# Optimization experiments

Measured on AMD Instinct MI355X. Metric: run time of the kernel, lower is better.

Reference implementation:

```python
import math
import jax, jax.numpy as jnp
import numpy as np

B, S, HID = 1, 256, 1024
H, D = 16, 64
INV_NORM = 1.0 / math.sqrt(D)  # inv_norm_factor (beta = 1.0)
NEG = -1e9


def _bloom_alibi(num_heads, seq_len):
    # standard Bloom alibi slopes, shape [H, 1, S]
    closest_pow2 = 2 ** math.floor(math.log2(num_heads))
    base = 2.0 ** (-(2.0 ** -(math.log2(closest_pow2) - 3)))
    slopes = base ** np.arange(1, closest_pow2 + 1)
    if closest_pow2 != num_heads:
        extra_base = 2.0 ** (-(2.0 ** -(math.log2(2 * closest_pow2) - 3)))
        n_extra = min(closest_pow2, num_heads - closest_pow2)
        slopes = np.concatenate([slopes, extra_base ** np.arange(1, 1 + 2 * n_extra, 2)])
    pos = np.arange(seq_len, dtype=np.float32)[None, None, :]
    return jnp.asarray(slopes[:, None, None].astype(np.float32) * pos)  # [H,1,S]


def setup_inputs() -> dict:
    key = jax.random.key(0)
    ks = jax.random.split(key, 6)
    hidden_states = jax.random.normal(ks[0], (B, S, HID), jnp.float32)
    residual = jax.random.normal(ks[1], (B, S, HID), jnp.float32)
    alibi = _bloom_alibi(H, S)  # [B*H, 1, S] with B=1
    # additive causal mask [B, 1, S, S]
    causal = jnp.tril(jnp.ones((S, S), bool))
    attention_mask = jnp.where(causal, 0.0, NEG).astype(jnp.float32)[None, None]
    W_qkv = jax.random.normal(ks[2], (HID, 3 * HID), jnp.float32) * (1.0 / math.sqrt(HID))
    b_qkv = jax.random.normal(ks[3], (3 * HID,), jnp.float32) * 0.02
    W_dense = jax.random.normal(ks[4], (HID, HID), jnp.float32) * (1.0 / math.sqrt(HID))
    b_dense = jax.random.normal(ks[5], (HID,), jnp.float32) * 0.02
    return dict(hidden_states=hidden_states, residual=residual, alibi=alibi,
                attention_mask=attention_mask, W_qkv=W_qkv, b_qkv=b_qkv,
                W_dense=W_dense, b_dense=b_dense)


def reference(hidden_states, residual, alibi, attention_mask, W_qkv, b_qkv, W_dense, b_dense):
    b, s, _ = hidden_states.shape
    # fused qkv projection, Bloom layout: (B, S, H, 3, D)
    fused = (hidden_states @ W_qkv + b_qkv).reshape(b, s, H, 3, D)
    q = fused[..., 0, :].transpose(0, 2, 1, 3)  # [B,H,S,D]
    k = fused[..., 1, :].transpose(0, 2, 1, 3)
    v = fused[..., 2, :].transpose(0, 2, 1, 3)

    alibi_b = alibi.reshape(b, H, 1, s)  # broadcast over query dim
    # standard alibi attention scores: [B,H,S,S]
    scores = alibi_b + INV_NORM * jnp.einsum('bhid,bhjd->bhij', q, k)
    scores = scores + attention_mask  # mask applied only to full scores (as in source)
    # per-dim delta scores: [B,H,D,S,S]; delta[b,h,d,i,j] = alibi + inv_norm * q_d * k_d
    delta = alibi_b[:, :, None] + INV_NORM * jnp.einsum('bhid,bhjd->bhdij', q, k)

    diff = (scores[:, :, None] - delta) * (1.0 / math.sqrt(D))
    p_diff = jax.nn.softmax(diff.astype(jnp.float32), axis=-1)  # [B,H,D,S,S]
    p = jax.nn.softmax(scores.astype(jnp.float32), axis=-1)     # [B,H,S,S]

    # qk importance: sum over batch, query, key of squared deviation, per (h, d)
    qk_importance = jnp.sum((p_diff - p[:, :, None]) ** 2, axis=(0, 3, 4)).reshape(-1)  # [H*D]

    context = jnp.einsum('bhij,bhjd->bhid', p, v)  # [B,H,S,D]
    context = context.transpose(0, 2, 1, 3).reshape(b, s, H * D)
    out = context @ W_dense + b_dense
    out = out + residual  # eval mode: dropout is identity
    return out, qk_importance
```

## Files before the change

kernel.cpp:

```cpp
#include <hip/hip_runtime.h>
#include <math.h>

#define NH  16
#define SEQ 256
#define HD  64
#define HID 1024
#define N3  3072

#define OFF_QB   0
#define OFF_KB   131072
#define OFF_KTB  262144
#define OFF_VTB  393216
#define OFF_CTX  524288

typedef __attribute__((ext_vector_type(8))) short bf16x8;
typedef __attribute__((ext_vector_type(4))) float f32x4;
typedef __attribute__((ext_vector_type(2))) unsigned short us2;
typedef __attribute__((ext_vector_type(4))) unsigned short us4;
typedef __attribute__((ext_vector_type(8))) unsigned short us8;

__device__ __forceinline__ unsigned short f2bf(float x) {
  unsigned u = __builtin_bit_cast(unsigned, x);
  u += 0x7FFF + ((u >> 16) & 1);
  return (unsigned short)(u >> 16);
}
__device__ __forceinline__ float bf2f(unsigned short b) {
  return __builtin_bit_cast(float, (unsigned)b << 16);
}

__global__ __launch_bounds__(256) void k_qkv(
    const float* __restrict__ A, const float* __restrict__ W,
    const float* __restrict__ bias, float* __restrict__ ws,
    float* __restrict__ out) {
  if (blockIdx.x == 0 && blockIdx.y < 4)
    out[SEQ * HID + blockIdx.y * 256 + threadIdx.x] = 0.f;
  __shared__ __align__(16) unsigned short As[32 * 72];
  __shared__ __align__(16) unsigned short Bs[32 * 72];
  const int tid = threadIdx.x;
  const int w = tid >> 6, lane = tid & 63;
  const int col = lane & 15, quad = lane >> 4;
  const int m0 = blockIdx.y * 32, n0 = blockIdx.x * 32;
  const int am = tid >> 3, ak = (tid & 7) * 8;
  const int bn = tid & 31, bkg = (tid >> 5) * 8;
  const float* Wp = W + n0 + bn;
  float4 a0 = *(const float4*)&A[(m0 + am) * HID + ak];
  float4 a1 = *(const float4*)&A[(m0 + am) * HID + ak + 4];
  float pb[8];
#pragma unroll
  for (int u = 0; u < 8; ++u) pb[u] = Wp[(bkg + u) * N3];
  f32x4 acc = {0.f, 0.f, 0.f, 0.f};
  const int k8 = quad * 8;
  const int mt = w & 1, nt = w >> 1;
  for (int k0 = 0; k0 < HID; k0 += 64) {
    *(us8*)&As[am * 72 + ak] =
        (us8){f2bf(a0.x), f2bf(a0.y), f2bf(a0.z), f2bf(a0.w),
              f2bf(a1.x), f2bf(a1.y), f2bf(a1.z), f2bf(a1.w)};
    us8 bp;
#pragma unroll
    for (int u = 0; u < 8; ++u) bp[u] = f2bf(pb[u]);
    *(us8*)&Bs[bn * 72 + bkg] = bp;
    __syncthreads();
    const int kn = k0 + 64;
    if (kn < HID) {
      a0 = *(const float4*)&A[(m0 + am) * HID + kn + ak];
      a1 = *(const float4*)&A[(m0 + am) * HID + kn + ak + 4];
#pragma unroll
      for (int u = 0; u < 8; ++u) pb[u] = Wp[(kn + bkg + u) * N3];
    }
    const bf16x8 af0 = *(const bf16x8*)&As[(mt * 16 + col) * 72 + k8];
    const bf16x8 af1 = *(const bf16x8*)&As[(mt * 16 + col) * 72 + k8 + 32];
    const bf16x8 bf0 = *(const bf16x8*)&Bs[(nt * 16 + col) * 72 + k8];
    const bf16x8 bf1 = *(const bf16x8*)&Bs[(nt * 16 + col) * 72 + k8 + 32];
    acc = __builtin_amdgcn_mfma_f32_16x16x32_bf16(af0, bf0, acc, 0, 0, 0);
    acc = __builtin_amdgcn_mfma_f32_16x16x32_bf16(af1, bf1, acc, 0, 0, 0);
    __syncthreads();
  }
  unsigned short* qb  = (unsigned short*)(ws + OFF_QB);
  unsigned short* kb  = (unsigned short*)(ws + OFF_KB);
  unsigned short* ktb = (unsigned short*)(ws + OFF_KTB);
  unsigned short* vtb = (unsigned short*)(ws + OFF_VTB);
  const int n = n0 + nt * 16 + col;
  const int h = n / 192;
  const int r2 = n - h * 192;
  const int which = r2 >> 6, d = r2 & 63;
  const float bv = bias[n];
#pragma unroll
  for (int r = 0; r < 4; ++r) {
    const int m = m0 + mt * 16 + quad * 4 + r;
    const unsigned short vb = f2bf(acc[r] + bv);
    if (which == 0) {
      qb[(h * SEQ + m) * HD + d] = vb;
    } else if (which == 1) {
      kb[(h * SEQ + m) * HD + d] = vb;
      ktb[(h * HD + d) * SEQ + m] = vb;
    } else {
      vtb[(h * HD + d) * SEQ + m] = vb;
    }
  }
}

__global__ __launch_bounds__(256) void k_attn(
    const float* __restrict__ alibi, float* __restrict__ ws,
    float* __restrict__ out) {
  *(float4*)&out[(blockIdx.x * 256 + threadIdx.x) * 4] =
      (float4){0.f, 0.f, 0.f, 0.f};
  const int bx = blockIdx.x;
  const int h = bx >> 4, i0 = (bx & 15) * 16;
  const int tid = threadIdx.x, w = tid >> 6, lane = tid & 63;
  const int col = lane & 15, quad = lane >> 4;
  __shared__ __align__(16) unsigned short Albs[3 * 16 * 280];
  __shared__ __align__(16) float plds[16 * 260];
  __shared__ __align__(16) float redm[16][4];
  __shared__ __align__(16) float reds[16][4];
  __shared__ __align__(16) float red4[16][4][4];
  __shared__ __align__(16) float rowsc[16][4];
  const unsigned short* qbh  = (const unsigned short*)(ws + OFF_QB) + h * SEQ * HD;
  const unsigned short* kbh  = (const unsigned short*)(ws + OFF_KB) + h * SEQ * HD;
  const unsigned short* ktbh = (const unsigned short*)(ws + OFF_KTB) + h * HD * SEQ;
  const unsigned short* vtbh = (const unsigned short*)(ws + OFF_VTB) + h * HD * SEQ;
  const bf16x8 a0 = *(const bf16x8*)&qbh[(i0 + col) * HD + quad * 8];
  const bf16x8 a1 = *(const bf16x8*)&qbh[(i0 + col) * HD + quad * 8 + 32];
  f32x4 acc[4] = {{0.f, 0.f, 0.f, 0.f}, {0.f, 0.f, 0.f, 0.f},
                  {0.f, 0.f, 0.f, 0.f}, {0.f, 0.f, 0.f, 0.f}};
#pragma unroll
  for (int t = 0; t < 4; ++t) {
    const int j = w * 64 + t * 16 + col;
    const bf16x8 b0 = *(const bf16x8*)&kbh[j * HD + quad * 8];
    const bf16x8 b1 = *(const bf16x8*)&kbh[j * HD + quad * 8 + 32];
    acc[t] = __builtin_amdgcn_mfma_f32_16x16x32_bf16(a0, b0, acc[t], 0, 0, 0);
    acc[t] = __builtin_amdgcn_mfma_f32_16x16x32_bf16(a1, b1, acc[t], 0, 0, 0);
  }
  float c[4][4], eb[4][4];
  float rmax[4] = {-3.0e38f, -3.0e38f, -3.0e38f, -3.0e38f};
#pragma unroll
  for (int t = 0; t < 4; ++t) {
    const int j = w * 64 + t * 16 + col;
    const float al = alibi[h * SEQ + j];
#pragma unroll
    for (int r = 0; r < 4; ++r) {
      const int i = i0 + quad * 4 + r;
      const float s = acc[t][r] * 0.125f;
      const float mv = (j <= i) ? 0.f : -1e9f;
      eb[t][r] = __expf((s + mv) * 0.125f);
      const float cv = al + s + mv;
      c[t][r] = cv;
      rmax[r] = fmaxf(rmax[r], cv);
    }
  }
#pragma unroll
  for (int r = 0; r < 4; ++r)
#pragma unroll
    for (int off = 1; off < 16; off <<= 1)
      rmax[r] = fmaxf(rmax[r], __shfl_xor(rmax[r], off));
  if (col == 0)
#pragma unroll
    for (int r = 0; r < 4; ++r) redm[quad * 4 + r][w] = rmax[r];
  __syncthreads();
  float rsum[4];
#pragma unroll
  for (int r = 0; r < 4; ++r) {
    const float4 m4 = *(const float4*)redm[quad * 4 + r];
    const float M = fmaxf(fmaxf(m4.x, m4.y), fmaxf(m4.z, m4.w));
    float s = 0.f;
#pragma unroll
    for (int t = 0; t < 4; ++t) {
      c[t][r] = __expf(c[t][r] - M);
      s += c[t][r];
    }
#pragma unroll
    for (int off = 1; off < 16; off <<= 1) s += __shfl_xor(s, off);
    rsum[r] = s;
  }
  if (col == 0)
#pragma unroll
    for (int r = 0; r < 4; ++r) reds[quad * 4 + r][w] = rsum[r];
  __syncthreads();
#pragma unroll
  for (int r = 0; r < 4; ++r) {
    const float4 s4 = *(const float4*)reds[quad * 4 + r];
    const float inv = __builtin_amdgcn_rcpf((s4.x + s4.y) + (s4.z + s4.w));
    const int il = quad * 4 + r;
    float s0 = 0.f, t0 = 0.f, u0 = 0.f, sp = 0.f;
#pragma unroll
    for (int t = 0; t < 4; ++t) {
      const int j = w * 64 + t * 16 + col;
      const float p = c[t][r] * inv;
      const float E = eb[t][r];
      plds[il * 260 + j] = p;
      Albs[il * 280 + j] = f2bf(E);
      Albs[16 * 280 + il * 280 + j] = f2bf(E * E);
      Albs[2 * 16 * 280 + il * 280 + j] = f2bf(E * p);
      s0 += E;
      t0 = __builtin_fmaf(E, E, t0);
      u0 = __builtin_fmaf(E, p, u0);
      sp = __builtin_fmaf(p, p, sp);
    }
#pragma unroll
    for (int off = 1; off < 16; off <<= 1) {
      s0 += __shfl_xor(s0, off);
      t0 += __shfl_xor(t0, off);
      u0 += __shfl_xor(u0, off);
      sp += __shfl_xor(sp, off);
    }
    if (col == 0) *(float4*)&red4[il][w][0] = (float4){s0, t0, u0, sp};
  }
  __syncthreads();
  if (tid < 64) {
    const int row = tid >> 2, x = tid & 3;
    rowsc[row][x] = (red4[row][0][x] + red4[row][1][x]) +
                    (red4[row][2][x] + red4[row][3][x]);
  }
  __syncthreads();
  f32x4 o = {0.f, 0.f, 0.f, 0.f};
#pragma unroll
  for (int s = 0; s < 8; ++s) {
    const int kk = quad * 8 + s * 32;
    const float4 pa = *(const float4*)&plds[col * 260 + kk];
    const float4 pc = *(const float4*)&plds[col * 260 + kk + 4];
    const us8 af = {f2bf(pa.x), f2bf(pa.y), f2bf(pa.z), f2bf(pa.w),
                    f2bf(pc.x), f2bf(pc.y), f2bf(pc.z), f2bf(pc.w)};
    const bf16x8 vb = *(const bf16x8*)&vtbh[(w * 16 + col) * SEQ + kk];
    o = __builtin_amdgcn_mfma_f32_16x16x32_bf16(
        __builtin_bit_cast(bf16x8, af), vb, o, 0, 0, 0);
  }
  float* ctx = ws + OFF_CTX;
#pragma unroll
  for (int r = 0; r < 4; ++r)
    ctx[(i0 + quad * 4 + r) * HID + h * HD + w * 16 + col] = o[r];
  f32x4 m6[3][2] = {{{0.f, 0.f, 0.f, 0.f}, {0.f, 0.f, 0.f, 0.f}},
                    {{0.f, 0.f, 0.f, 0.f}, {0.f, 0.f, 0.f, 0.f}},
                    {{0.f, 0.f, 0.f, 0.f}, {0.f, 0.f, 0.f, 0.f}}};
  const unsigned short* ktrow = ktbh + (w * 16 + col) * SEQ;
#pragma unroll
  for (int s = 0; s < 8; ++s) {
    const int kk = quad * 8 + s * 32;
    const bf16x8 kb8 = *(const bf16x8*)&ktrow[kk];
    us8 kq;
#pragma unroll
    for (int u = 0; u < 8; ++u) {
      const float t = bf2f((unsigned short)kb8[u]);
      kq[u] = f2bf(t * t);
    }
    const bf16x8 k2 = __builtin_bit_cast(bf16x8, kq);
#pragma unroll
    for (int lhs = 0; lhs < 3; ++lhs) {
      const bf16x8 af = *(const bf16x8*)&Albs[lhs * 16 * 280 + col * 280 + kk];
      m6[lhs][0] = __builtin_amdgcn_mfma_f32_16x16x32_bf16(af, kb8, m6[lhs][0], 0, 0, 0);
      m6[lhs][1] = __builtin_amdgcn_mfma_f32_16x16x32_bf16(af, k2, m6[lhs][1], 0, 0, 0);
    }
  }
  const int dg = w * 16 + col;
  float racc = 0.f;
#pragma unroll
  for (int r = 0; r < 4; ++r) {
    const int il = quad * 4 + r;
    const float qc = -0.015625f * bf2f(qbh[(i0 + il) * HD + dg]);
    const float s0 = rowsc[il][0], t0 = rowsc[il][1];
    const float u0 = rowsc[il][2], sp = rowsc[il][3];
    const float S1 = __builtin_fmaf(
        qc, __builtin_fmaf(0.5f * qc, m6[0][1][r], m6[0][0][r]), s0);
    const float S2 = __builtin_fmaf(
        2.f * qc, __builtin_fmaf(qc, m6[1][1][r], m6[1][0][r]), t0);
    const float S3 = __builtin_fmaf(
        qc, __builtin_fmaf(0.5f * qc, m6[2][1][r], m6[2][0][r]), u0);
    const float inv = __builtin_amdgcn_rcpf(S1);
    racc += __builtin_fmaf(__builtin_fmaf(S2, inv, -2.f * S3), inv, sp);
  }
  racc += __shfl_xor(racc, 16);
  racc += __shfl_xor(racc, 32);
  if (lane < 16) atomicAdd(&out[SEQ * HID + h * HD + w * 16 + lane], racc);
}

__global__ __launch_bounds__(256) void k_dense(
    const float* __restrict__ W, const float* __restrict__ bias,
    const float* __restrict__ resid, float* __restrict__ out,
    const float* __restrict__ ws) {
  __shared__ __align__(16) unsigned short As[16 * 72];
  __shared__ __align__(16) unsigned short Bs[64 * 72];
  const int tid = threadIdx.x;
  const int w = tid >> 6, lane = tid & 63;
  const int col = lane & 15, quad = lane >> 4;
  const int m0 = blockIdx.y * 16, n0 = blockIdx.x * 64;
  const int kb = blockIdx.z * 256;
  const int am = tid >> 4, ak = (tid & 15) * 4;
  const int bkg = w * 16;
  const float* A = ws + OFF_CTX;
  const float* Wp = W + n0 + lane;
  float4 a0 = *(const float4*)&A[(m0 + am) * HID + kb + ak];
  float pb[16];
#pragma unroll
  for (int u = 0; u < 16; ++u) pb[u] = Wp[(kb + bkg + u) * HID];
  f32x4 acc = {0.f, 0.f, 0.f, 0.f};
  const int k8 = quad * 8;
  for (int k0 = 0; k0 < 256; k0 += 64) {
    *(us4*)&As[am * 72 + ak] =
        (us4){f2bf(a0.x), f2bf(a0.y), f2bf(a0.z), f2bf(a0.w)};
    us8 bp0, bp1;
#pragma unroll
    for (int u = 0; u < 8; ++u) { bp0[u] = f2bf(pb[u]); bp1[u] = f2bf(pb[u + 8]); }
    *(us8*)&Bs[lane * 72 + bkg] = bp0;
    *(us8*)&Bs[lane * 72 + bkg + 8] = bp1;
    __syncthreads();
    const int kn = k0 + 64;
    if (kn < 256) {
      a0 = *(const float4*)&A[(m0 + am) * HID + kb + kn + ak];
#pragma unroll
      for (int u = 0; u < 16; ++u) pb[u] = Wp[(kb + kn + bkg + u) * HID];
    }
    const bf16x8 af0 = *(const bf16x8*)&As[col * 72 + k8];
    const bf16x8 af1 = *(const bf16x8*)&As[col * 72 + k8 + 32];
    const bf16x8 bf0 = *(const bf16x8*)&Bs[(w * 16 + col) * 72 + k8];
    const bf16x8 bf1 = *(const bf16x8*)&Bs[(w * 16 + col) * 72 + k8 + 32];
    acc = __builtin_amdgcn_mfma_f32_16x16x32_bf16(af0, bf0, acc, 0, 0, 0);
    acc = __builtin_amdgcn_mfma_f32_16x16x32_bf16(af1, bf1, acc, 0, 0, 0);
    __syncthreads();
  }
  const int n = n0 + w * 16 + col;
  const bool first = (blockIdx.z == 0);
  const float bv = first ? bias[n] : 0.f;
#pragma unroll
  for (int r = 0; r < 4; ++r) {
    const int m = m0 + quad * 4 + r;
    const float v = acc[r] + (first ? bv + resid[m * HID + n] : 0.f);
    atomicAdd(&out[m * HID + n], v);
  }
}

extern "C" void kernel_launch(void* const* d_in, const int* in_sizes, int n_in,
                              void* d_out, int out_size, void* d_ws,
                              size_t ws_size, hipStream_t stream) {
  const float* hidden   = (const float*)d_in[0];
  const float* residual = (const float*)d_in[1];
  const float* alibi    = (const float*)d_in[2];
  const float* Wqkv     = (const float*)d_in[4];
  const float* bqkv     = (const float*)d_in[5];
  const float* Wd       = (const float*)d_in[6];
  const float* bd       = (const float*)d_in[7];
  float* out = (float*)d_out;
  float* ws  = (float*)d_ws;

  k_qkv<<<dim3(96, 8), 256, 0, stream>>>(hidden, Wqkv, bqkv, ws, out);
  k_attn<<<dim3(256), 256, 0, stream>>>(alibi, ws, out);
  k_dense<<<dim3(16, 16, 4), 256, 0, stream>>>(Wd, bd, residual, out, ws);
}
```

Baseline: 107.6 us.

## Double-buffer GEMM prefetch, use packed bf16 converts, store P and context as bf16

The QKV and dense GEMMs now keep two k-tiles of global loads in flight, alternating register sets, so each load has more time to land before it is used. All float-to-bf16 conversions switch from software rounding to the packed v_cvt_pk_bf16_f32 instruction. The attention kernel stores the probability tile in LDS as bf16 instead of fp32, and it writes the context to the workspace as bf16, which halves the dense kernel's A-operand reads. The price is higher register pressure from the doubled prefetch buffers and an extra rounding of the context, though the dense kernel already rounded it to bf16 before.

```diff
diff --git a/kernel.cpp b/kernel.cpp
--- a/kernel.cpp
+++ b/kernel.cpp
@@ -18,6 +18,7 @@
 typedef __attribute__((ext_vector_type(2))) unsigned short us2;
 typedef __attribute__((ext_vector_type(4))) unsigned short us4;
 typedef __attribute__((ext_vector_type(8))) unsigned short us8;
+typedef __attribute__((ext_vector_type(4))) unsigned u32x4;
 
 __device__ __forceinline__ unsigned short f2bf(float x) {
   unsigned u = __builtin_bit_cast(unsigned, x);
@@ -26,6 +27,11 @@
 }
 __device__ __forceinline__ float bf2f(unsigned short b) {
   return __builtin_bit_cast(float, (unsigned)b << 16);
+}
+__device__ __forceinline__ unsigned f2bf2(float lo, float hi) {
+  unsigned r;
+  asm("v_cvt_pk_bf16_f32 %0, %1, %2" : "=v"(r) : "v"(lo), "v"(hi));
+  return r;
 }
 
 __global__ __launch_bounds__(256) void k_qkv(
@@ -42,37 +48,67 @@
   const int m0 = blockIdx.y * 32, n0 = blockIdx.x * 32;
   const int am = tid >> 3, ak = (tid & 7) * 8;
   const int bn = tid & 31, bkg = (tid >> 5) * 8;
+  const float* Ap = &A[(m0 + am) * HID + ak];
   const float* Wp = W + n0 + bn;
-  float4 a0 = *(const float4*)&A[(m0 + am) * HID + ak];
-  float4 a1 = *(const float4*)&A[(m0 + am) * HID + ak + 4];
-  float pb[8];
-#pragma unroll
-  for (int u = 0; u < 8; ++u) pb[u] = Wp[(bkg + u) * N3];
+  float4 a0 = *(const float4*)&Ap[0];
+  float4 a1 = *(const float4*)&Ap[4];
+  float pa[8];
+#pragma unroll
+  for (int u = 0; u < 8; ++u) pa[u] = Wp[(bkg + u) * N3];
+  float4 c0 = *(const float4*)&Ap[64];
+  float4 c1 = *(const float4*)&Ap[68];
+  float pc[8];
+#pragma unroll
+  for (int u = 0; u < 8; ++u) pc[u] = Wp[(64 + bkg + u) * N3];
   f32x4 acc = {0.f, 0.f, 0.f, 0.f};
   const int k8 = quad * 8;
   const int mt = w & 1, nt = w >> 1;
-  for (int k0 = 0; k0 < HID; k0 += 64) {
-    *(us8*)&As[am * 72 + ak] =
-        (us8){f2bf(a0.x), f2bf(a0.y), f2bf(a0.z), f2bf(a0.w),
-              f2bf(a1.x), f2bf(a1.y), f2bf(a1.z), f2bf(a1.w)};
-    us8 bp;
-#pragma unroll
-    for (int u = 0; u < 8; ++u) bp[u] = f2bf(pb[u]);
-    *(us8*)&Bs[bn * 72 + bkg] = bp;
-    __syncthreads();
-    const int kn = k0 + 64;
-    if (kn < HID) {
-      a0 = *(const float4*)&A[(m0 + am) * HID + kn + ak];
-      a1 = *(const float4*)&A[(m0 + am) * HID + kn + ak + 4];
-#pragma unroll
-      for (int u = 0; u < 8; ++u) pb[u] = Wp[(kn + bkg + u) * N3];
-    }
-    const bf16x8 af0 = *(const bf16x8*)&As[(mt * 16 + col) * 72 + k8];
-    const bf16x8 af1 = *(const bf16x8*)&As[(mt * 16 + col) * 72 + k8 + 32];
-    const bf16x8 bf0 = *(const bf16x8*)&Bs[(nt * 16 + col) * 72 + k8];
-    const bf16x8 bf1 = *(const bf16x8*)&Bs[(nt * 16 + col) * 72 + k8 + 32];
-    acc = __builtin_amdgcn_mfma_f32_16x16x32_bf16(af0, bf0, acc, 0, 0, 0);
-    acc = __builtin_amdgcn_mfma_f32_16x16x32_bf16(af1, bf1, acc, 0, 0, 0);
+  for (int k0 = 0; k0 < HID; k0 += 128) {
+    *(u32x4*)&As[am * 72 + ak] =
+        (u32x4){f2bf2(a0.x, a0.y), f2bf2(a0.z, a0.w),
+                f2bf2(a1.x, a1.y), f2bf2(a1.z, a1.w)};
+    *(u32x4*)&Bs[bn * 72 + bkg] =
+        (u32x4){f2bf2(pa[0], pa[1]), f2bf2(pa[2], pa[3]),
+                f2bf2(pa[4], pa[5]), f2bf2(pa[6], pa[7])};
+    __syncthreads();
+    const int ka = k0 + 128;
+    if (ka < HID) {
+      a0 = *(const float4*)&Ap[ka];
+      a1 = *(const float4*)&Ap[ka + 4];
+#pragma unroll
+      for (int u = 0; u < 8; ++u) pa[u] = Wp[(ka + bkg + u) * N3];
+    }
+    {
+      const bf16x8 af0 = *(const bf16x8*)&As[(mt * 16 + col) * 72 + k8];
+      const bf16x8 af1 = *(const bf16x8*)&As[(mt * 16 + col) * 72 + k8 + 32];
+      const bf16x8 bf0 = *(const bf16x8*)&Bs[(nt * 16 + col) * 72 + k8];
+      const bf16x8 bf1 = *(const bf16x8*)&Bs[(nt * 16 + col) * 72 + k8 + 32];
+      acc = __builtin_amdgcn_mfma_f32_16x16x32_bf16(af0, bf0, acc, 0, 0, 0);
+      acc = __builtin_amdgcn_mfma_f32_16x16x32_bf16(af1, bf1, acc, 0, 0, 0);
+    }
+    __syncthreads();
+    *(u32x4*)&As[am * 72 + ak] =
+        (u32x4){f2bf2(c0.x, c0.y), f2bf2(c0.z, c0.w),
+                f2bf2(c1.x, c1.y), f2bf2(c1.z, c1.w)};
+    *(u32x4*)&Bs[bn * 72 + bkg] =
+        (u32x4){f2bf2(pc[0], pc[1]), f2bf2(pc[2], pc[3]),
+                f2bf2(pc[4], pc[5]), f2bf2(pc[6], pc[7])};
+    __syncthreads();
+    const int kb2 = k0 + 192;
+    if (kb2 < HID) {
+      c0 = *(const float4*)&Ap[kb2];
+      c1 = *(const float4*)&Ap[kb2 + 4];
+#pragma unroll
+      for (int u = 0; u < 8; ++u) pc[u] = Wp[(kb2 + bkg + u) * N3];
+    }
+    {
+      const bf16x8 af0 = *(const bf16x8*)&As[(mt * 16 + col) * 72 + k8];
+      const bf16x8 af1 = *(const bf16x8*)&As[(mt * 16 + col) * 72 + k8 + 32];
+      const bf16x8 bf0 = *(const bf16x8*)&Bs[(nt * 16 + col) * 72 + k8];
+      const bf16x8 bf1 = *(const bf16x8*)&Bs[(nt * 16 + col) * 72 + k8 + 32];
+      acc = __builtin_amdgcn_mfma_f32_16x16x32_bf16(af0, bf0, acc, 0, 0, 0);
+      acc = __builtin_amdgcn_mfma_f32_16x16x32_bf16(af1, bf1, acc, 0, 0, 0);
+    }
     __syncthreads();
   }
   unsigned short* qb  = (unsigned short*)(ws + OFF_QB);
@@ -84,10 +120,15 @@
   const int r2 = n - h * 192;
   const int which = r2 >> 6, d = r2 & 63;
   const float bv = bias[n];
+  const unsigned v01 = f2bf2(acc[0] + bv, acc[1] + bv);
+  const unsigned v23 = f2bf2(acc[2] + bv, acc[3] + bv);
+  const unsigned short vbr[4] = {
+      (unsigned short)v01, (unsigned short)(v01 >> 16),
+      (unsigned short)v23, (unsigned short)(v23 >> 16)};
 #pragma unroll
   for (int r = 0; r < 4; ++r) {
     const int m = m0 + mt * 16 + quad * 4 + r;
-    const unsigned short vb = f2bf(acc[r] + bv);
+    const unsigned short vb = vbr[r];
     if (which == 0) {
       qb[(h * SEQ + m) * HD + d] = vb;
     } else if (which == 1) {
@@ -109,7 +150,7 @@
   const int tid = threadIdx.x, w = tid >> 6, lane = tid & 63;
   const int col = lane & 15, quad = lane >> 4;
   __shared__ __align__(16) unsigned short Albs[3 * 16 * 280];
-  __shared__ __align__(16) float plds[16 * 260];
+  __shared__ __align__(16) unsigned short plds[16 * 272];
   __shared__ __align__(16) float redm[16][4];
   __shared__ __align__(16) float reds[16][4];
   __shared__ __align__(16) float red4[16][4][4];
@@ -180,21 +221,37 @@
     const float4 s4 = *(const float4*)reds[quad * 4 + r];
     const float inv = __builtin_amdgcn_rcpf((s4.x + s4.y) + (s4.z + s4.w));
     const int il = quad * 4 + r;
+    float pt[4];
     float s0 = 0.f, t0 = 0.f, u0 = 0.f, sp = 0.f;
 #pragma unroll
     for (int t = 0; t < 4; ++t) {
-      const int j = w * 64 + t * 16 + col;
       const float p = c[t][r] * inv;
       const float E = eb[t][r];
-      plds[il * 260 + j] = p;
-      Albs[il * 280 + j] = f2bf(E);
-      Albs[16 * 280 + il * 280 + j] = f2bf(E * E);
-      Albs[2 * 16 * 280 + il * 280 + j] = f2bf(E * p);
+      pt[t] = p;
       s0 += E;
       t0 = __builtin_fmaf(E, E, t0);
       u0 = __builtin_fmaf(E, p, u0);
       sp = __builtin_fmaf(p, p, sp);
     }
+    const int jb = il * 280 + w * 64 + col;
+    const int pb = il * 272 + w * 64 + col;
+    unsigned x;
+    x = f2bf2(eb[0][r], eb[1][r]);
+    Albs[jb] = (unsigned short)x; Albs[jb + 16] = (unsigned short)(x >> 16);
+    x = f2bf2(eb[2][r], eb[3][r]);
+    Albs[jb + 32] = (unsigned short)x; Albs[jb + 48] = (unsigned short)(x >> 16);
+    x = f2bf2(eb[0][r] * eb[0][r], eb[1][r] * eb[1][r]);
+    Albs[4480 + jb] = (unsigned short)x; Albs[4480 + jb + 16] = (unsigned short)(x >> 16);
+    x = f2bf2(eb[2][r] * eb[2][r], eb[3][r] * eb[3][r]);
+    Albs[4480 + jb + 32] = (unsigned short)x; Albs[4480 + jb + 48] = (unsigned short)(x >> 16);
+    x = f2bf2(eb[0][r] * pt[0], eb[1][r] * pt[1]);
+    Albs[8960 + jb] = (unsigned short)x; Albs[8960 + jb + 16] = (unsigned short)(x >> 16);
+    x = f2bf2(eb[2][r] * pt[2], eb[3][r] * pt[3]);
+    Albs[8960 + jb + 32] = (unsigned short)x; Albs[8960 + jb + 48] = (unsigned short)(x >> 16);
+    x = f2bf2(pt[0], pt[1]);
+    plds[pb] = (unsigned short)x; plds[pb + 16] = (unsigned short)(x >> 16);
+    x = f2bf2(pt[2], pt[3]);
+    plds[pb + 32] = (unsigned short)x; plds[pb + 48] = (unsigned short)(x >> 16);
 #pragma unroll
     for (int off = 1; off < 16; off <<= 1) {
       s0 += __shfl_xor(s0, off);
@@ -215,18 +272,20 @@
 #pragma unroll
   for (int s = 0; s < 8; ++s) {
     const int kk = quad * 8 + s * 32;
-    const float4 pa = *(const float4*)&plds[col * 260 + kk];
-    const float4 pc = *(const float4*)&plds[col * 260 + kk + 4];
-    const us8 af = {f2bf(pa.x), f2bf(pa.y), f2bf(pa.z), f2bf(pa.w),
-                    f2bf(pc.x), f2bf(pc.y), f2bf(pc.z), f2bf(pc.w)};
+    const bf16x8 pa8 = *(const bf16x8*)&plds[col * 272 + kk];
     const bf16x8 vb = *(const bf16x8*)&vtbh[(w * 16 + col) * SEQ + kk];
-    o = __builtin_amdgcn_mfma_f32_16x16x32_bf16(
-        __builtin_bit_cast(bf16x8, af), vb, o, 0, 0, 0);
-  }
-  float* ctx = ws + OFF_CTX;
-#pragma unroll
-  for (int r = 0; r < 4; ++r)
-    ctx[(i0 + quad * 4 + r) * HID + h * HD + w * 16 + col] = o[r];
+    o = __builtin_amdgcn_mfma_f32_16x16x32_bf16(pa8, vb, o, 0, 0, 0);
+  }
+  unsigned short* ctxb = (unsigned short*)(ws + OFF_CTX);
+  {
+    const unsigned x01 = f2bf2(o[0], o[1]);
+    const unsigned x23 = f2bf2(o[2], o[3]);
+    const int cb = h * HD + w * 16 + col;
+    ctxb[(i0 + quad * 4 + 0) * HID + cb] = (unsigned short)x01;
+    ctxb[(i0 + quad * 4 + 1) * HID + cb] = (unsigned short)(x01 >> 16);
+    ctxb[(i0 + quad * 4 + 2) * HID + cb] = (unsigned short)x23;
+    ctxb[(i0 + quad * 4 + 3) * HID + cb] = (unsigned short)(x23 >> 16);
+  }
   f32x4 m6[3][2] = {{{0.f, 0.f, 0.f, 0.f}, {0.f, 0.f, 0.f, 0.f}},
                     {{0.f, 0.f, 0.f, 0.f}, {0.f, 0.f, 0.f, 0.f}},
                     {{0.f, 0.f, 0.f, 0.f}, {0.f, 0.f, 0.f, 0.f}}};
@@ -235,16 +294,17 @@
   for (int s = 0; s < 8; ++s) {
     const int kk = quad * 8 + s * 32;
     const bf16x8 kb8 = *(const bf16x8*)&ktrow[kk];
-    us8 kq;
-#pragma unroll
-    for (int u = 0; u < 8; ++u) {
-      const float t = bf2f((unsigned short)kb8[u]);
-      kq[u] = f2bf(t * t);
-    }
-    const bf16x8 k2 = __builtin_bit_cast(bf16x8, kq);
+    u32x4 kq4;
+#pragma unroll
+    for (int u = 0; u < 4; ++u) {
+      const float t0 = bf2f((unsigned short)kb8[2 * u]);
+      const float t1 = bf2f((unsigned short)kb8[2 * u + 1]);
+      kq4[u] = f2bf2(t0 * t0, t1 * t1);
+    }
+    const bf16x8 k2 = __builtin_bit_cast(bf16x8, kq4);
 #pragma unroll
     for (int lhs = 0; lhs < 3; ++lhs) {
-      const bf16x8 af = *(const bf16x8*)&Albs[lhs * 16 * 280 + col * 280 + kk];
+      const bf16x8 af = *(const bf16x8*)&Albs[lhs * 4480 + col * 280 + kk];
       m6[lhs][0] = __builtin_amdgcn_mfma_f32_16x16x32_bf16(af, kb8, m6[lhs][0], 0, 0, 0);
       m6[lhs][1] = __builtin_amdgcn_mfma_f32_16x16x32_bf16(af, k2, m6[lhs][1], 0, 0, 0);
     }
@@ -284,35 +344,65 @@
   const int kb = blockIdx.z * 256;
   const int am = tid >> 4, ak = (tid & 15) * 4;
   const int bkg = w * 16;
-  const float* A = ws + OFF_CTX;
+  const unsigned short* Ab = (const unsigned short*)(ws + OFF_CTX);
+  const unsigned short* Ap = &Ab[(m0 + am) * HID + kb + ak];
   const float* Wp = W + n0 + lane;
-  float4 a0 = *(const float4*)&A[(m0 + am) * HID + kb + ak];
-  float pb[16];
-#pragma unroll
-  for (int u = 0; u < 16; ++u) pb[u] = Wp[(kb + bkg + u) * HID];
+  us4 aA = *(const us4*)&Ap[0];
+  float pA[16];
+#pragma unroll
+  for (int u = 0; u < 16; ++u) pA[u] = Wp[(kb + bkg + u) * HID];
+  us4 aB = *(const us4*)&Ap[64];
+  float pB[16];
+#pragma unroll
+  for (int u = 0; u < 16; ++u) pB[u] = Wp[(kb + 64 + bkg + u) * HID];
   f32x4 acc = {0.f, 0.f, 0.f, 0.f};
   const int k8 = quad * 8;
-  for (int k0 = 0; k0 < 256; k0 += 64) {
-    *(us4*)&As[am * 72 + ak] =
-        (us4){f2bf(a0.x), f2bf(a0.y), f2bf(a0.z), f2bf(a0.w)};
-    us8 bp0, bp1;
-#pragma unroll
-    for (int u = 0; u < 8; ++u) { bp0[u] = f2bf(pb[u]); bp1[u] = f2bf(pb[u + 8]); }
-    *(us8*)&Bs[lane * 72 + bkg] = bp0;
-    *(us8*)&Bs[lane * 72 + bkg + 8] = bp1;
-    __syncthreads();
-    const int kn = k0 + 64;
-    if (kn < 256) {
-      a0 = *(const float4*)&A[(m0 + am) * HID + kb + kn + ak];
-#pragma unroll
-      for (int u = 0; u < 16; ++u) pb[u] = Wp[(kb + kn + bkg + u) * HID];
-    }
-    const bf16x8 af0 = *(const bf16x8*)&As[col * 72 + k8];
-    const bf16x8 af1 = *(const bf16x8*)&As[col * 72 + k8 + 32];
-    const bf16x8 bf0 = *(const bf16x8*)&Bs[(w * 16 + col) * 72 + k8];
-    const bf16x8 bf1 = *(const bf16x8*)&Bs[(w * 16 + col) * 72 + k8 + 32];
-    acc = __builtin_amdgcn_mfma_f32_16x16x32_bf16(af0, bf0, acc, 0, 0, 0);
-    acc = __builtin_amdgcn_mfma_f32_16x16x32_bf16(af1, bf1, acc, 0, 0, 0);
+  for (int k0 = 0; k0 < 256; k0 += 128) {
+    *(us4*)&As[am * 72 + ak] = aA;
+    *(u32x4*)&Bs[lane * 72 + bkg] =
+        (u32x4){f2bf2(pA[0], pA[1]), f2bf2(pA[2], pA[3]),
+                f2bf2(pA[4], pA[5]), f2bf2(pA[6], pA[7])};
+    *(u32x4*)&Bs[lane * 72 + bkg + 8] =
+        (u32x4){f2bf2(pA[8], pA[9]), f2bf2(pA[10], pA[11]),
+                f2bf2(pA[12], pA[13]), f2bf2(pA[14], pA[15])};
+    __syncthreads();
+    const int ka = k0 + 128;
+    if (ka < 256) {
+      aA = *(const us4*)&Ap[ka];
+#pragma unroll
+      for (int u = 0; u < 16; ++u) pA[u] = Wp[(kb + ka + bkg + u) * HID];
+    }
+    {
+      const bf16x8 af0 = *(const bf16x8*)&As[col * 72 + k8];
+      const bf16x8 af1 = *(const bf16x8*)&As[col * 72 + k8 + 32];
+      const bf16x8 bf0 = *(const bf16x8*)&Bs[(w * 16 + col) * 72 + k8];
+      const bf16x8 bf1 = *(const bf16x8*)&Bs[(w * 16 + col) * 72 + k8 + 32];
+      acc = __builtin_amdgcn_mfma_f32_16x16x32_bf16(af0, bf0, acc, 0, 0, 0);
+      acc = __builtin_amdgcn_mfma_f32_16x16x32_bf16(af1, bf1, acc, 0, 0, 0);
+    }
+    __syncthreads();
+    *(us4*)&As[am * 72 + ak] = aB;
+    *(u32x4*)&Bs[lane * 72 + bkg] =
+        (u32x4){f2bf2(pB[0], pB[1]), f2bf2(pB[2], pB[3]),
+                f2bf2(pB[4], pB[5]), f2bf2(pB[6], pB[7])};
+    *(u32x4*)&Bs[lane * 72 + bkg + 8] =
+        (u32x4){f2bf2(pB[8], pB[9]), f2bf2(pB[10], pB[11]),
+                f2bf2(pB[12], pB[13]), f2bf2(pB[14], pB[15])};
+    __syncthreads();
+    const int kb2 = k0 + 192;
+    if (kb2 < 256) {
+      aB = *(const us4*)&Ap[kb2];
+#pragma unroll
+      for (int u = 0; u < 16; ++u) pB[u] = Wp[(kb + kb2 + bkg + u) * HID];
+    }
+    {
+      const bf16x8 af0 = *(const bf16x8*)&As[col * 72 + k8];
+      const bf16x8 af1 = *(const bf16x8*)&As[col * 72 + k8 + 32];
+      const bf16x8 bf0 = *(const bf16x8*)&Bs[(w * 16 + col) * 72 + k8];
+      const bf16x8 bf1 = *(const bf16x8*)&Bs[(w * 16 + col) * 72 + k8 + 32];
+      acc = __builtin_amdgcn_mfma_f32_16x16x32_bf16(af0, bf0, acc, 0, 0, 0);
+      acc = __builtin_amdgcn_mfma_f32_16x16x32_bf16(af1, bf1, acc, 0, 0, 0);
+    }
     __syncthreads();
   }
   const int n = n0 + w * 16 + col;
```

Measured after the change: 104.9 us. 2.6% less time.
